# Optimization experiments

Measured on AMD Instinct MI355X. Metric: run time of the kernel, lower is better.

Reference implementation:

```python
import jax, jax.numpy as jnp
import numpy as np

BATCH, SEQ, DIM = 4, 4096, 256
DT_RANK, D_STATE, NUM_TOKENS = 16, 16, 1024


def _adapool(x, T):
    # uniform window mean == AdaptiveAvgPool1d when S % T == 0
    B, S, D = x.shape
    return x.reshape(B, T, S // T, D).mean(axis=2)


def _layernorm(x, g, b, eps=1e-5):
    mu = x.mean(-1, keepdims=True)
    var = ((x - mu) ** 2).mean(-1, keepdims=True)
    return (x - mu) * jax.lax.rsqrt(var + eps) * g + b


def _gauss_mask(T):
    c = (T + 1) // 2
    idx = jnp.arange(T, dtype=jnp.float32)
    sigma = jnp.abs(idx - c).mean()
    w = jnp.exp(-0.5 * (idx - c) ** 2 / sigma ** 2)
    return w / w.sum()


def _ssm(x, Wdbc, Wdt, bdt, Alog, D):
    A = -jnp.exp(Alog)                                     # (Dm, N)
    dbc = x @ Wdbc.T                                       # (B,L,dt+2N)
    delta = jax.nn.softplus(dbc[..., :DT_RANK] @ Wdt.T + bdt)   # (B,L,Dm)
    Bm = dbc[..., DT_RANK:DT_RANK + D_STATE]               # (B,L,N)
    Cm = dbc[..., DT_RANK + D_STATE:]                      # (B,L,N)
    deltaA = jnp.exp(delta[..., None] * A)                 # (B,L,Dm,N)
    BX = (delta[..., None] * Bm[:, :, None, :]) * x[..., None]
    def comb(c1, c2):
        a1, x1 = c1
        a2, x2 = c2
        return (a2 * a1, a2 * x1 + x2)
    _, hs = jax.lax.associative_scan(comb, (deltaA, BX), axis=1)
    y = jnp.einsum('bldn,bln->bld', hs, Cm) + D * x
    return y


def setup_inputs():
    key = jax.random.key(0)
    ks = jax.random.split(key, 16)
    s = 0.05
    Alog = jnp.tile(jnp.log(jnp.arange(1.0, D_STATE + 1.0, dtype=jnp.float32))[None, :], (DIM, 1))
    return {
        'x': jax.random.normal(ks[0], (BATCH, SEQ, DIM), jnp.float32),
        'ln_g': jnp.ones((DIM,), jnp.float32),
        'ln_b': jnp.zeros((DIM,), jnp.float32),
        'W1': jax.random.normal(ks[1], (DIM, DIM), jnp.float32) * s,
        'b1': jnp.zeros((DIM,), jnp.float32),
        'W2': jax.random.normal(ks[2], (DIM, DIM), jnp.float32) * s,
        'b2': jnp.zeros((DIM,), jnp.float32),
        'Wcf': jax.random.normal(ks[3], (DIM, DIM), jnp.float32) * s,
        'bcf': jnp.zeros((DIM,), jnp.float32),
        'Wcb': jax.random.normal(ks[4], (DIM, DIM), jnp.float32) * s,
        'bcb': jnp.zeros((DIM,), jnp.float32),
        'Wdbc_f': jax.random.normal(ks[5], (DT_RANK + 2 * D_STATE, DIM), jnp.float32) * s,
        'Wdt_f': jax.random.normal(ks[6], (DIM, DT_RANK), jnp.float32) * s,
        'bdt_f': jnp.zeros((DIM,), jnp.float32),
        'Alog_f': Alog,
        'D_f': jnp.ones((DIM,), jnp.float32),
        'Wdbc_b': jax.random.normal(ks[7], (DT_RANK + 2 * D_STATE, DIM), jnp.float32) * s,
        'Wdt_b': jax.random.normal(ks[8], (DIM, DT_RANK), jnp.float32) * s,
        'bdt_b': jnp.zeros((DIM,), jnp.float32),
        'Alog_b': Alog,
        'D_b': jnp.ones((DIM,), jnp.float32),
    }


def reference(x, ln_g, ln_b, W1, b1, W2, b2, Wcf, bcf, Wcb, bcb,
              Wdbc_f, Wdt_f, bdt_f, Alog_f, D_f,
              Wdbc_b, Wdt_b, bdt_b, Alog_b, D_b):
    skip = _adapool(x, NUM_TOKENS)
    xn = _layernorm(x, ln_g, ln_b)
    z = xn @ W1.T + b1
    xp = xn @ W2.T + b2
    mask = _gauss_mask(NUM_TOKENS)[None, :, None]

    # forward direction: 1x1 conv (= channel linear) -> softplus -> SSM
    h1 = jax.nn.softplus(jnp.einsum('bsd,ed->bse', xp, Wcf) + bcf)
    x1 = _ssm(h1, Wdbc_f, Wdt_f, bdt_f, Alog_f, D_f)
    x1 = jax.nn.silu(_adapool(x1, NUM_TOKENS) * mask)

    # backward direction on flipped sequence
    h2 = jax.nn.softplus(jnp.einsum('bsd,ed->bse', xp[:, ::-1], Wcb) + bcb)
    x2 = _ssm(h2, Wdbc_b, Wdt_b, bdt_b, Alog_b, D_b)[:, ::-1]
    x2 = jax.nn.silu(_adapool(x2, NUM_TOKENS) * mask)

    zp = jax.nn.silu(_adapool(z, NUM_TOKENS))
    return zp * x1 + zp * x2 + skip
```

## Files before the change

### kernel.cpp

```cpp
#include <hip/hip_runtime.h>
#include <math.h>


namespace {
constexpr int BB = 4;
constexpr int LL = 4096;
constexpr int DD = 256;
constexpr int NS = 16;
constexpr int NCH = 64;
constexpr int CLEN = 64;
constexpr int TOK = 1024;

constexpr size_t NROW = (size_t)BB * LL;
constexpr size_t NE   = NROW * DD;
constexpr size_t NP   = (size_t)BB * TOK * DD;
constexpr size_t NBC  = NROW * NS;
constexpr size_t NAGG = 2ull * BB * DD * NCH * NS;

constexpr size_t O_XN   = 0;
constexpr size_t O_DLF  = O_XN;
constexpr size_t O_DLB  = NE / 2;
constexpr size_t O_H1X  = NE;
constexpr size_t O_G2X  = NE + NE / 2;
constexpr size_t O_BMF  = 2 * NE;
constexpr size_t O_CMF  = O_BMF + NBC / 2;
constexpr size_t O_BMB  = O_CMF + NBC / 2;
constexpr size_t O_CMB  = O_BMB + NBC / 2;
constexpr size_t O_ZP   = O_CMB + NBC / 2;
constexpr size_t O_SKIP = O_ZP + NP;
constexpr size_t O_Y1   = O_SKIP + NP;
constexpr size_t O_Y2   = O_Y1 + NP;
constexpr size_t O_WF1  = O_Y2 + NP;
constexpr size_t O_BF1  = O_WF1 + 768 * 256 / 2;
constexpr size_t O_WF2F = O_BF1 + 768;
constexpr size_t O_B2F  = O_WF2F + 384 * 256 / 2;
constexpr size_t O_WF2B = O_B2F + 384;
constexpr size_t O_B2B  = O_WF2B + 384 * 256 / 2;
constexpr size_t O_APROD = O_B2B + 384;
constexpr size_t O_HEND = O_APROD + NAGG;
constexpr size_t O_MASK = O_HEND + NAGG;
}

typedef __bf16 bf16x8 __attribute__((ext_vector_type(8)));
typedef float f32x4 __attribute__((ext_vector_type(4)));

__device__ __forceinline__ float softplusf(float x) {
    return fmaxf(x, 0.f) + __logf(1.f + __expf(-fabsf(x)));
}
__device__ __forceinline__ float siluf(float x) {
    return x / (1.f + __expf(-x));
}
__device__ __forceinline__ void gl_lds16(const void* g, void* l) {
    __builtin_amdgcn_global_load_lds((const __attribute__((address_space(1))) unsigned int*)g,
                                     (__attribute__((address_space(3))) unsigned int*)l, 16, 0, 0);
}
__device__ __forceinline__ void pow_chain(float e1, float* p) {
    p[0] = e1;
    p[1] = e1 * e1;
    p[2] = p[1] * e1;
    p[3] = p[1] * p[1];
    p[4] = p[3] * p[0];
    p[5] = p[3] * p[1];
    p[6] = p[3] * p[2];
    p[7] = p[3] * p[3];
    p[8]  = p[7] * p[0];
    p[9]  = p[7] * p[1];
    p[10] = p[7] * p[2];
    p[11] = p[7] * p[3];
    p[12] = p[7] * p[4];
    p[13] = p[7] * p[5];
    p[14] = p[7] * p[6];
    p[15] = p[7] * p[7];
}

__global__ __launch_bounds__(256) void prep_wc_kernel(
    const float* __restrict__ W1, const float* __restrict__ b1,
    const float* __restrict__ W2, const float* __restrict__ b2,
    const float* __restrict__ Wcf, const float* __restrict__ bcf,
    const float* __restrict__ Wcb, const float* __restrict__ bcb,
    __bf16* __restrict__ Wf1, float* __restrict__ bf1)
{
    int j = blockIdx.x, mat = blockIdx.y, k = threadIdx.x;
    const float* Wc = mat ? Wcb : Wcf;
    float acc = 0.f, accb = 0.f;
    for (int m = 0; m < 256; ++m) {
        float w = Wc[j * 256 + m];
        acc  = fmaf(w, W2[m * 256 + k], acc);
        accb = fmaf(w, b2[m], accb);
    }
    Wf1[(size_t)(256 + mat * 256 + j) * 256 + k] = (__bf16)acc;
    if (k == 0) bf1[256 + mat * 256 + j] = accb + (mat ? bcb[j] : bcf[j]);
    if (mat == 0) {
        Wf1[(size_t)j * 256 + k] = (__bf16)W1[j * 256 + k];
        if (k == 0) bf1[j] = b1[j];
    }
}

__global__ __launch_bounds__(256) void prep_wdd_kernel(
    const float* __restrict__ Wdt_f, const float* __restrict__ Wdbc_f, const float* __restrict__ bdt_f,
    const float* __restrict__ Wdt_b, const float* __restrict__ Wdbc_b, const float* __restrict__ bdt_b,
    __bf16* __restrict__ Wf2f, float* __restrict__ b2f,
    __bf16* __restrict__ Wf2b, float* __restrict__ b2b)
{
    int j = blockIdx.x, mat = blockIdx.y, k = threadIdx.x;
    const float* Wdt  = mat ? Wdt_b : Wdt_f;
    const float* Wdbc = mat ? Wdbc_b : Wdbc_f;
    const float* bdt  = mat ? bdt_b : bdt_f;
    __bf16* Wf2 = mat ? Wf2b : Wf2f;
    float* b2x  = mat ? b2b : b2f;
    float val;
    if (j < 256) {
        float acc = 0.f;
#pragma unroll
        for (int m = 0; m < 16; ++m)
            acc = fmaf(Wdt[j * 16 + m], Wdbc[m * 256 + k], acc);
        val = acc;
    } else if (j < 288) {
        val = Wdbc[(16 + (j - 256)) * 256 + k];
    } else {
        val = 0.f;
    }
    Wf2[(size_t)j * 256 + k] = (__bf16)val;
    if (k == 0) b2x[j] = (j < 256) ? bdt[j] : 0.f;
}

__global__ __launch_bounds__(1024) void mask_kernel(float* __restrict__ mask)
{
    __shared__ float red[16];
    __shared__ float bc;
    int t = threadIdx.x;
    const float c = 512.f;
    float ft = (float)t;
    float v = fabsf(ft - c);
    for (int o = 32; o > 0; o >>= 1) v += __shfl_xor(v, o, 64);
    if ((t & 63) == 0) red[t >> 6] = v;
    __syncthreads();
    if (t == 0) { float s = 0; for (int i = 0; i < 16; ++i) s += red[i]; bc = s * (1.f / 1024.f); }
    __syncthreads();
    float sigma = bc;
    float w = __expf(-0.5f * (ft - c) * (ft - c) / (sigma * sigma));
    v = w;
    for (int o = 32; o > 0; o >>= 1) v += __shfl_xor(v, o, 64);
    if ((t & 63) == 0) red[t >> 6] = v;
    __syncthreads();
    if (t == 0) { float s = 0; for (int i = 0; i < 16; ++i) s += red[i]; bc = s; }
    __syncthreads();
    mask[t] = w / bc;
}

__global__ __launch_bounds__(256) void ln_kernel(
    const float* __restrict__ x, const float* __restrict__ lng, const float* __restrict__ lnb,
    __bf16* __restrict__ xn, float* __restrict__ skipo)
{
    __shared__ float red[8];
    __shared__ float mv[2];
    int t = threadIdx.x;
    int r0 = blockIdx.x * 4;
    float gg = lng[t], bbv = lnb[t];
    float acc = 0.f;
    for (int i = 0; i < 4; ++i) {
        size_t r = r0 + i;
        float v = x[r * 256 + t];
        float s = v, q = v * v;
        for (int o = 32; o > 0; o >>= 1) { s += __shfl_xor(s, o, 64); q += __shfl_xor(q, o, 64); }
        if ((t & 63) == 0) { red[t >> 6] = s; red[4 + (t >> 6)] = q; }
        __syncthreads();
        if (t == 0) {
            float S = red[0] + red[1] + red[2] + red[3];
            float Q = red[4] + red[5] + red[6] + red[7];
            float mu = S * (1.f / 256.f);
            mv[0] = mu;
            mv[1] = rsqrtf(Q * (1.f / 256.f) - mu * mu + 1e-5f);
        }
        __syncthreads();
        xn[r * 256 + t] = (__bf16)((v - mv[0]) * mv[1] * gg + bbv);
        acc += v;
        __syncthreads();
    }
    int b = r0 >> 12;
    int g = (r0 & 4095) >> 2;
    skipo[((size_t)b * TOK + g) * 256 + t] = acc * 0.25f;
}

__global__ __launch_bounds__(256) void gemm1_mfma(
    const __bf16* __restrict__ A, const __bf16* __restrict__ Bw, const float* __restrict__ bias,
    float* __restrict__ zp, __bf16* __restrict__ h1x, __bf16* __restrict__ g2x)
{
    __shared__ __align__(16) __bf16 As[4096];
    __shared__ __align__(16) __bf16 Bs[4096];
    int tid = threadIdx.x;
    int lane = tid & 63, wv = tid >> 6;
    int wr = wv >> 1, wc = wv & 1;
    int lm = lane & 15, lq = lane >> 4;
    int m0 = blockIdx.x << 7, n0 = blockIdx.y << 7;

    const __bf16* ga0 = A  + (size_t)(m0 + wv * 32 + lm) * 256 + lq * 8;
    const __bf16* ga1 = ga0 + 16 * 256;
    const __bf16* gb0 = Bw + (size_t)(n0 + wv * 32 + lm) * 256 + lq * 8;
    const __bf16* gb1 = gb0 + 16 * 256;
    __bf16* la0 = &As[(wv * 2    ) * 512];
    __bf16* la1 = &As[(wv * 2 + 1) * 512];
    __bf16* lb0 = &Bs[(wv * 2    ) * 512];
    __bf16* lb1 = &Bs[(wv * 2 + 1) * 512];

    f32x4 acc[4][4];
#pragma unroll
    for (int i = 0; i < 4; ++i)
#pragma unroll
        for (int j = 0; j < 4; ++j) acc[i][j] = 0;

    for (int k0 = 0; k0 < 256; k0 += 32) {
        __syncthreads();
        gl_lds16(ga0 + k0, la0);
        gl_lds16(ga1 + k0, la1);
        gl_lds16(gb0 + k0, lb0);
        gl_lds16(gb1 + k0, lb1);
        __syncthreads();
        bf16x8 af[4], bfr[4];
#pragma unroll
        for (int i = 0; i < 4; ++i)
            af[i] = *(const bf16x8*)&As[(wr * 4 + i) * 512 + lane * 8];
#pragma unroll
        for (int j = 0; j < 4; ++j)
            bfr[j] = *(const bf16x8*)&Bs[(wc * 4 + j) * 512 + lane * 8];
#pragma unroll
        for (int i = 0; i < 4; ++i)
#pragma unroll
            for (int j = 0; j < 4; ++j)
                acc[i][j] = __builtin_amdgcn_mfma_f32_16x16x32_bf16(af[i], bfr[j], acc[i][j], 0, 0, 0);
    }

    int target = blockIdx.y >> 1;
    if (target == 0) {
#pragma unroll
        for (int j = 0; j < 4; ++j) {
            int col = n0 + wc * 64 + j * 16 + lm;
            float bv = bias[col];
#pragma unroll
            for (int i = 0; i < 4; ++i) {
                int row0 = m0 + wr * 64 + i * 16 + lq * 4;
                float s = acc[i][j][0] + acc[i][j][1] + acc[i][j][2] + acc[i][j][3];
                float zv = siluf(0.25f * s + bv);
                int b = row0 >> 12, g = (row0 & 4095) >> 2;
                zp[((size_t)b * TOK + g) * 256 + col] = zv;
            }
        }
    } else {
        __bf16* outp = (target == 1) ? h1x : g2x;
#pragma unroll
        for (int j = 0; j < 4; ++j) {
            int col = n0 + wc * 64 + j * 16 + lm;
            float bv = bias[col];
            int cl = col & 255;
#pragma unroll
            for (int i = 0; i < 4; ++i) {
                int row = m0 + wr * 64 + i * 16 + lq * 4;
#pragma unroll
                for (int r = 0; r < 4; ++r) {
                    float v = acc[i][j][r] + bv;
                    outp[(size_t)(row + r) * 256 + cl] = (__bf16)softplusf(v);
                }
            }
        }
    }
}

__global__ __launch_bounds__(256) void gemm2_mfma(
    const __bf16* __restrict__ h1x, const __bf16* __restrict__ g2x,
    const __bf16* __restrict__ Wf, const float* __restrict__ bf2,
    const __bf16* __restrict__ Wb, const float* __restrict__ bb2,
    __bf16* __restrict__ dlf, __bf16* __restrict__ dlb,
    __bf16* __restrict__ BmF, __bf16* __restrict__ CmF,
    __bf16* __restrict__ BmB, __bf16* __restrict__ CmB)
{
    __shared__ __align__(16) __bf16 As[4096];
    __shared__ __align__(16) __bf16 Bs[4096];
    int tid = threadIdx.x;
    int lane = tid & 63, wv = tid >> 6;
    int wr = wv >> 1, wc = wv & 1;
    int lm = lane & 15, lq = lane >> 4;
    int m0 = blockIdx.x << 7, n0 = blockIdx.y << 7;
    int dir = blockIdx.z;
    const __bf16* A    = dir ? g2x : h1x;
    const __bf16* Bw   = dir ? Wb : Wf;
    const float* bias  = dir ? bb2 : bf2;
    __bf16* dl = dir ? dlb : dlf;
    __bf16* Bm = dir ? BmB : BmF;
    __bf16* Cm = dir ? CmB : CmF;

    const __bf16* ga0 = A  + (size_t)(m0 + wv * 32 + lm) * 256 + lq * 8;
    const __bf16* ga1 = ga0 + 16 * 256;
    const __bf16* gb0 = Bw + (size_t)(n0 + wv * 32 + lm) * 256 + lq * 8;
    const __bf16* gb1 = gb0 + 16 * 256;
    __bf16* la0 = &As[(wv * 2    ) * 512];
    __bf16* la1 = &As[(wv * 2 + 1) * 512];
    __bf16* lb0 = &Bs[(wv * 2    ) * 512];
    __bf16* lb1 = &Bs[(wv * 2 + 1) * 512];

    f32x4 acc[4][4];
#pragma unroll
    for (int i = 0; i < 4; ++i)
#pragma unroll
        for (int j = 0; j < 4; ++j) acc[i][j] = 0;

    for (int k0 = 0; k0 < 256; k0 += 32) {
        __syncthreads();
        gl_lds16(ga0 + k0, la0);
        gl_lds16(ga1 + k0, la1);
        gl_lds16(gb0 + k0, lb0);
        gl_lds16(gb1 + k0, lb1);
        __syncthreads();
        bf16x8 af[4], bfr[4];
#pragma unroll
        for (int i = 0; i < 4; ++i)
            af[i] = *(const bf16x8*)&As[(wr * 4 + i) * 512 + lane * 8];
#pragma unroll
        for (int j = 0; j < 4; ++j)
            bfr[j] = *(const bf16x8*)&Bs[(wc * 4 + j) * 512 + lane * 8];
#pragma unroll
        for (int i = 0; i < 4; ++i)
#pragma unroll
            for (int j = 0; j < 4; ++j)
                acc[i][j] = __builtin_amdgcn_mfma_f32_16x16x32_bf16(af[i], bfr[j], acc[i][j], 0, 0, 0);
    }

#pragma unroll
    for (int j = 0; j < 4; ++j) {
        int col = n0 + wc * 64 + j * 16 + lm;
        if (col >= 288) continue;
        float bv = bias[col];
#pragma unroll
        for (int i = 0; i < 4; ++i) {
            int row = m0 + wr * 64 + i * 16 + lq * 4;
#pragma unroll
            for (int r = 0; r < 4; ++r) {
                float v = acc[i][j][r] + bv;
                size_t rr = (size_t)(row + r);
                if (col < 256)       dl[rr * 256 + col] = (__bf16)softplusf(v);
                else if (col < 272)  Bm[rr * 16 + (col - 256)] = (__bf16)v;
                else                 Cm[rr * 16 + (col - 272)] = (__bf16)v;
            }
        }
    }
}

__global__ __launch_bounds__(256) void scan1_kernel(
    const __bf16* __restrict__ df, const __bf16* __restrict__ db,
    const __bf16* __restrict__ xf, const __bf16* __restrict__ xb,
    const __bf16* __restrict__ bmf, const __bf16* __restrict__ bmb,
    const float* __restrict__ alogf, const float* __restrict__ alogb,
    float* __restrict__ aprod, float* __restrict__ hend)
{
    int d = threadIdx.x;
    int c = blockIdx.x, b = blockIdx.y, dir = blockIdx.z;
    const __bf16* delta = dir ? db : df;
    const __bf16* xin   = dir ? xb : xf;
    const __bf16* Bm    = dir ? bmb : bmf;
    const float* Alog   = dir ? alogb : alogf;

    float A[16];
    bool intOK = true;
#pragma unroll
    for (int n = 0; n < 16; ++n) {
        A[n] = -__expf(Alog[(size_t)d * 16 + n]);
        intOK = intOK && (fabsf(A[n] + (float)(n + 1)) < 1e-3f);
    }
    float h[16];
#pragma unroll
    for (int n = 0; n < 16; ++n) h[n] = 0.f;
    float sd = 0.f;
    int base = c * CLEN;
    if (intOK) {
        for (int it = 0; it < CLEN; ++it) {
            int t = dir ? (base + CLEN - 1 - it) : (base + it);
            size_t row = (size_t)b * LL + t;
            float dlt = (float)delta[row * DD + d];
            float xv  = (float)xin[row * DD + d];
            float common = dlt * xv;
            sd += dlt;
            float p[16];
            pow_chain(__expf(-dlt), p);
            const bf16x8* Bp = (const bf16x8*)&Bm[row * NS];
            bf16x8 b0 = Bp[0], b1 = Bp[1];
#pragma unroll
            for (int n = 0; n < 8; ++n) {
                h[n]     = fmaf(p[n],     h[n],     common * (float)b0[n]);
                h[n + 8] = fmaf(p[n + 8], h[n + 8], common * (float)b1[n]);
            }
        }
        float pe[16];
        pow_chain(__expf(-sd), pe);
        size_t idx = ((((size_t)dir * BB + b) * DD + d) * NCH + c) * NS;
#pragma unroll
        for (int q = 0; q < 4; ++q) {
            float4 av, hv;
            av.x = pe[q * 4 + 0]; av.y = pe[q * 4 + 1]; av.z = pe[q * 4 + 2]; av.w = pe[q * 4 + 3];
            hv.x = h[q * 4 + 0];  hv.y = h[q * 4 + 1];  hv.z = h[q * 4 + 2];  hv.w = h[q * 4 + 3];
            *(float4*)&aprod[idx + q * 4] = av;
            *(float4*)&hend[idx + q * 4] = hv;
        }
    } else {
        for (int it = 0; it < CLEN; ++it) {
            int t = dir ? (base + CLEN - 1 - it) : (base + it);
            size_t row = (size_t)b * LL + t;
            float dlt = (float)delta[row * DD + d];
            float xv  = (float)xin[row * DD + d];
            float common = dlt * xv;
            sd += dlt;
            const bf16x8* Bp = (const bf16x8*)&Bm[row * NS];
            bf16x8 b0 = Bp[0], b1 = Bp[1];
#pragma unroll
            for (int n = 0; n < 8; ++n) {
                h[n]     = fmaf(__expf(dlt * A[n]),     h[n],     common * (float)b0[n]);
                h[n + 8] = fmaf(__expf(dlt * A[n + 8]), h[n + 8], common * (float)b1[n]);
            }
        }
        size_t idx = ((((size_t)dir * BB + b) * DD + d) * NCH + c) * NS;
#pragma unroll
        for (int n = 0; n < 16; ++n) {
            aprod[idx + n] = __expf(sd * A[n]);
            hend[idx + n] = h[n];
        }
    }
}

__global__ __launch_bounds__(256) void scan2_kernel(
    const float* __restrict__ aprod, float* __restrict__ hh)
{
    int g = blockIdx.x * 256 + threadIdx.x;
    int n = g & 15, d = (g >> 4) & 255, b = (g >> 12) & 3, dir = (g >> 14) & 1;
    size_t bidx = (((size_t)dir * BB + b) * DD + d) * NCH;
    float s = 0.f;
    if (!dir) {
        for (int c = 0; c < NCH; ++c) {
            size_t idx = (bidx + c) * NS + n;
            float a = aprod[idx], he = hh[idx];
            hh[idx] = s;
            s = fmaf(a, s, he);
        }
    } else {
        for (int c = NCH - 1; c >= 0; --c) {
            size_t idx = (bidx + c) * NS + n;
            float a = aprod[idx], he = hh[idx];
            hh[idx] = s;
            s = fmaf(a, s, he);
        }
    }
}

__global__ __launch_bounds__(256) void scan3_kernel(
    const __bf16* __restrict__ df, const __bf16* __restrict__ db,
    const __bf16* __restrict__ xf, const __bf16* __restrict__ xb,
    const __bf16* __restrict__ bmf, const __bf16* __restrict__ bmb,
    const __bf16* __restrict__ cmf, const __bf16* __restrict__ cmb,
    const float* __restrict__ alogf, const float* __restrict__ alogb,
    const float* __restrict__ Dfp, const float* __restrict__ Dbp,
    const float* __restrict__ hin,
    float* __restrict__ y1, float* __restrict__ y2)
{
    int d = threadIdx.x;
    int c = blockIdx.x, b = blockIdx.y, dir = blockIdx.z;
    const __bf16* delta = dir ? db : df;
    const __bf16* xin   = dir ? xb : xf;
    const __bf16* Bm    = dir ? bmb : bmf;
    const __bf16* Cm    = dir ? cmb : cmf;
    const float* Alog   = dir ? alogb : alogf;
    const float* Dv     = dir ? Dbp : Dfp;
    float* yout = dir ? y2 : y1;

    float A[16];
    bool intOK = true;
#pragma unroll
    for (int n = 0; n < 16; ++n) {
        A[n] = -__expf(Alog[(size_t)d * 16 + n]);
        intOK = intOK && (fabsf(A[n] + (float)(n + 1)) < 1e-3f);
    }
    float Dd = Dv[d];
    float h[16];
    size_t idx = ((((size_t)dir * BB + b) * DD + d) * NCH + c) * NS;
#pragma unroll
    for (int q = 0; q < 4; ++q) {
        float4 hv = *(const float4*)&hin[idx + q * 4];
        h[q * 4 + 0] = hv.x; h[q * 4 + 1] = hv.y; h[q * 4 + 2] = hv.z; h[q * 4 + 3] = hv.w;
    }
    int base = c * CLEN;
    float pool = 0.f;
    if (intOK) {
        for (int it = 0; it < CLEN; ++it) {
            int t = dir ? (base + CLEN - 1 - it) : (base + it);
            size_t row = (size_t)b * LL + t;
            float dlt = (float)delta[row * DD + d];
            float xv  = (float)xin[row * DD + d];
            float common = dlt * xv;
            float p[16];
            pow_chain(__expf(-dlt), p);
            const bf16x8* Bp = (const bf16x8*)&Bm[row * NS];
            const bf16x8* Cp = (const bf16x8*)&Cm[row * NS];
            bf16x8 b0 = Bp[0], b1 = Bp[1];
            bf16x8 c0 = Cp[0], c1 = Cp[1];
            float yac = 0.f;
#pragma unroll
            for (int n = 0; n < 8; ++n) {
                h[n]     = fmaf(p[n],     h[n],     common * (float)b0[n]);
                h[n + 8] = fmaf(p[n + 8], h[n + 8], common * (float)b1[n]);
                yac = fmaf(h[n], (float)c0[n], yac);
                yac = fmaf(h[n + 8], (float)c1[n], yac);
            }
            pool += yac + Dd * xv;
            bool gend = dir ? ((t & 3) == 0) : ((t & 3) == 3);
            if (gend) {
                yout[((size_t)b * TOK + (t >> 2)) * DD + d] = pool * 0.25f;
                pool = 0.f;
            }
        }
    } else {
        for (int it = 0; it < CLEN; ++it) {
            int t = dir ? (base + CLEN - 1 - it) : (base + it);
            size_t row = (size_t)b * LL + t;
            float dlt = (float)delta[row * DD + d];
            float xv  = (float)xin[row * DD + d];
            float common = dlt * xv;
            const bf16x8* Bp = (const bf16x8*)&Bm[row * NS];
            const bf16x8* Cp = (const bf16x8*)&Cm[row * NS];
            bf16x8 b0 = Bp[0], b1 = Bp[1];
            bf16x8 c0 = Cp[0], c1 = Cp[1];
            float yac = 0.f;
#pragma unroll
            for (int n = 0; n < 8; ++n) {
                h[n]     = fmaf(__expf(dlt * A[n]),     h[n],     common * (float)b0[n]);
                h[n + 8] = fmaf(__expf(dlt * A[n + 8]), h[n + 8], common * (float)b1[n]);
                yac = fmaf(h[n], (float)c0[n], yac);
                yac = fmaf(h[n + 8], (float)c1[n], yac);
            }
            pool += yac + Dd * xv;
            bool gend = dir ? ((t & 3) == 0) : ((t & 3) == 3);
            if (gend) {
                yout[((size_t)b * TOK + (t >> 2)) * DD + d] = pool * 0.25f;
                pool = 0.f;
            }
        }
    }
}

__global__ __launch_bounds__(256) void final_kernel(
    const float* __restrict__ zp, const float* __restrict__ y1, const float* __restrict__ y2,
    const float* __restrict__ mask, const float* __restrict__ skipi, float* __restrict__ out)
{
    int p = blockIdx.x;
    int g = p & 1023;
    int d = threadIdx.x;
    size_t ip = (size_t)p * 256 + d;
    float mk = mask[g];
    float a1 = y1[ip] * mk, a2 = y2[ip] * mk;
    out[ip] = zp[ip] * (siluf(a1) + siluf(a2)) + skipi[ip];
}

extern "C" void kernel_launch(void* const* d_in, const int* in_sizes, int n_in,
                              void* d_out, int out_size, void* d_ws, size_t ws_size,
                              hipStream_t stream)
{
    const float* x      = (const float*)d_in[0];
    const float* ln_g   = (const float*)d_in[1];
    const float* ln_b   = (const float*)d_in[2];
    const float* W1     = (const float*)d_in[3];
    const float* b1     = (const float*)d_in[4];
    const float* W2     = (const float*)d_in[5];
    const float* b2     = (const float*)d_in[6];
    const float* Wcf    = (const float*)d_in[7];
    const float* bcf    = (const float*)d_in[8];
    const float* Wcb    = (const float*)d_in[9];
    const float* bcb    = (const float*)d_in[10];
    const float* Wdbc_f = (const float*)d_in[11];
    const float* Wdt_f  = (const float*)d_in[12];
    const float* bdt_f  = (const float*)d_in[13];
    const float* Alog_f = (const float*)d_in[14];
    const float* D_f    = (const float*)d_in[15];
    const float* Wdbc_b = (const float*)d_in[16];
    const float* Wdt_b  = (const float*)d_in[17];
    const float* bdt_b  = (const float*)d_in[18];
    const float* Alog_b = (const float*)d_in[19];
    const float* D_b    = (const float*)d_in[20];
    float* out = (float*)d_out;
    float* ws  = (float*)d_ws;

    __bf16* xnb = (__bf16*)(ws + O_XN);
    __bf16* dlf = (__bf16*)(ws + O_DLF);
    __bf16* dlb = (__bf16*)(ws + O_DLB);
    __bf16* h1x = (__bf16*)(ws + O_H1X);
    __bf16* g2x = (__bf16*)(ws + O_G2X);
    __bf16* bmf = (__bf16*)(ws + O_BMF);
    __bf16* cmf = (__bf16*)(ws + O_CMF);
    __bf16* bmb = (__bf16*)(ws + O_BMB);
    __bf16* cmb = (__bf16*)(ws + O_CMB);
    float* zpb  = ws + O_ZP;
    float* skb  = ws + O_SKIP;
    float* y1b  = ws + O_Y1;
    float* y2b  = ws + O_Y2;
    __bf16* wf1 = (__bf16*)(ws + O_WF1);
    float* bf1  = ws + O_BF1;
    __bf16* wf2f = (__bf16*)(ws + O_WF2F);
    float* b2f  = ws + O_B2F;
    __bf16* wf2b = (__bf16*)(ws + O_WF2B);
    float* b2b  = ws + O_B2B;
    float* apr  = ws + O_APROD;
    float* hnd  = ws + O_HEND;
    float* mkb  = ws + O_MASK;

    prep_wc_kernel<<<dim3(256, 2), 256, 0, stream>>>(W1, b1, W2, b2, Wcf, bcf, Wcb, bcb, wf1, bf1);
    prep_wdd_kernel<<<dim3(384, 2), 256, 0, stream>>>(Wdt_f, Wdbc_f, bdt_f, Wdt_b, Wdbc_b, bdt_b,
                                                      wf2f, b2f, wf2b, b2b);
    mask_kernel<<<1, 1024, 0, stream>>>(mkb);
    ln_kernel<<<4096, 256, 0, stream>>>(x, ln_g, ln_b, xnb, skb);
    gemm1_mfma<<<dim3(128, 6), 256, 0, stream>>>(xnb, wf1, bf1, zpb, h1x, g2x);
    gemm2_mfma<<<dim3(128, 3, 2), 256, 0, stream>>>(h1x, g2x, wf2f, b2f, wf2b, b2b,
                                                    dlf, dlb, bmf, cmf, bmb, cmb);
    scan1_kernel<<<dim3(NCH, BB, 2), 256, 0, stream>>>(dlf, dlb, h1x, g2x, bmf, bmb,
                                                       Alog_f, Alog_b, apr, hnd);
    scan2_kernel<<<128, 256, 0, stream>>>(apr, hnd);
    scan3_kernel<<<dim3(NCH, BB, 2), 256, 0, stream>>>(dlf, dlb, h1x, g2x, bmf, bmb, cmf, cmb,
                                                       Alog_f, Alog_b, D_f, D_b, hnd, y1b, y2b);
    final_kernel<<<4096, 256, 0, stream>>>(zpb, y1b, y2b, mkb, skb, out);
}
```

Measured before the change: 252.2 us.

## Stage GEMM epilogues through LDS for vectorized stores and merge prep kernels

The GEMM1 and GEMM2 epilogues now write their activated results into a padded shared-memory staging tile and then store them to global memory as 16-byte vectors. This replaces the scattered per-element 2-byte and 4-byte stores that came straight out of the MFMA register layout. The three weight-prep and mask kernels are merged into one launch, with the Gaussian mask sigma folded into a constant. The scan2 loops are also unrolled. The extra shared memory per block can lower occupancy, and the staging adds extra barriers.

```diff
diff --git a/kernel.cpp b/kernel.cpp
--- a/kernel.cpp
+++ b/kernel.cpp
@@ -39,6 +39,8 @@
 constexpr size_t O_APROD = O_B2B + 384;
 constexpr size_t O_HEND = O_APROD + NAGG;
 constexpr size_t O_MASK = O_HEND + NAGG;
+
+constexpr int SSTRIDE = 136;
 }
 
 typedef __bf16 bf16x8 __attribute__((ext_vector_type(8)));
@@ -73,79 +75,75 @@
     p[15] = p[7] * p[7];
 }
 
-__global__ __launch_bounds__(256) void prep_wc_kernel(
+__global__ __launch_bounds__(256) void prep_all_kernel(
     const float* __restrict__ W1, const float* __restrict__ b1,
     const float* __restrict__ W2, const float* __restrict__ b2,
     const float* __restrict__ Wcf, const float* __restrict__ bcf,
     const float* __restrict__ Wcb, const float* __restrict__ bcb,
-    __bf16* __restrict__ Wf1, float* __restrict__ bf1)
-{
-    int j = blockIdx.x, mat = blockIdx.y, k = threadIdx.x;
-    const float* Wc = mat ? Wcb : Wcf;
-    float acc = 0.f, accb = 0.f;
-    for (int m = 0; m < 256; ++m) {
-        float w = Wc[j * 256 + m];
-        acc  = fmaf(w, W2[m * 256 + k], acc);
-        accb = fmaf(w, b2[m], accb);
-    }
-    Wf1[(size_t)(256 + mat * 256 + j) * 256 + k] = (__bf16)acc;
-    if (k == 0) bf1[256 + mat * 256 + j] = accb + (mat ? bcb[j] : bcf[j]);
-    if (mat == 0) {
-        Wf1[(size_t)j * 256 + k] = (__bf16)W1[j * 256 + k];
-        if (k == 0) bf1[j] = b1[j];
-    }
-}
-
-__global__ __launch_bounds__(256) void prep_wdd_kernel(
     const float* __restrict__ Wdt_f, const float* __restrict__ Wdbc_f, const float* __restrict__ bdt_f,
     const float* __restrict__ Wdt_b, const float* __restrict__ Wdbc_b, const float* __restrict__ bdt_b,
+    __bf16* __restrict__ Wf1, float* __restrict__ bf1,
     __bf16* __restrict__ Wf2f, float* __restrict__ b2f,
-    __bf16* __restrict__ Wf2b, float* __restrict__ b2b)
-{
-    int j = blockIdx.x, mat = blockIdx.y, k = threadIdx.x;
-    const float* Wdt  = mat ? Wdt_b : Wdt_f;
-    const float* Wdbc = mat ? Wdbc_b : Wdbc_f;
-    const float* bdt  = mat ? bdt_b : bdt_f;
-    __bf16* Wf2 = mat ? Wf2b : Wf2f;
-    float* b2x  = mat ? b2b : b2f;
-    float val;
-    if (j < 256) {
-        float acc = 0.f;
-#pragma unroll
-        for (int m = 0; m < 16; ++m)
-            acc = fmaf(Wdt[j * 16 + m], Wdbc[m * 256 + k], acc);
-        val = acc;
-    } else if (j < 288) {
-        val = Wdbc[(16 + (j - 256)) * 256 + k];
-    } else {
-        val = 0.f;
-    }
-    Wf2[(size_t)j * 256 + k] = (__bf16)val;
-    if (k == 0) b2x[j] = (j < 256) ? bdt[j] : 0.f;
-}
-
-__global__ __launch_bounds__(1024) void mask_kernel(float* __restrict__ mask)
-{
-    __shared__ float red[16];
-    __shared__ float bc;
-    int t = threadIdx.x;
-    const float c = 512.f;
-    float ft = (float)t;
-    float v = fabsf(ft - c);
-    for (int o = 32; o > 0; o >>= 1) v += __shfl_xor(v, o, 64);
-    if ((t & 63) == 0) red[t >> 6] = v;
-    __syncthreads();
-    if (t == 0) { float s = 0; for (int i = 0; i < 16; ++i) s += red[i]; bc = s * (1.f / 1024.f); }
-    __syncthreads();
-    float sigma = bc;
-    float w = __expf(-0.5f * (ft - c) * (ft - c) / (sigma * sigma));
-    v = w;
-    for (int o = 32; o > 0; o >>= 1) v += __shfl_xor(v, o, 64);
-    if ((t & 63) == 0) red[t >> 6] = v;
-    __syncthreads();
-    if (t == 0) { float s = 0; for (int i = 0; i < 16; ++i) s += red[i]; bc = s; }
-    __syncthreads();
-    mask[t] = w / bc;
+    __bf16* __restrict__ Wf2b, float* __restrict__ b2b,
+    float* __restrict__ mask)
+{
+    int bx = blockIdx.x, mat = blockIdx.y, k = threadIdx.x;
+    if (bx < 256) {
+        int j = bx;
+        const float* Wc = mat ? Wcb : Wcf;
+        float acc = 0.f, accb = 0.f;
+        for (int m = 0; m < 256; ++m) {
+            float w = Wc[j * 256 + m];
+            acc  = fmaf(w, W2[m * 256 + k], acc);
+            accb = fmaf(w, b2[m], accb);
+        }
+        Wf1[(size_t)(256 + mat * 256 + j) * 256 + k] = (__bf16)acc;
+        if (k == 0) bf1[256 + mat * 256 + j] = accb + (mat ? bcb[j] : bcf[j]);
+        if (mat == 0) {
+            Wf1[(size_t)j * 256 + k] = (__bf16)W1[j * 256 + k];
+            if (k == 0) bf1[j] = b1[j];
+        }
+    } else if (bx < 640) {
+        int j = bx - 256;
+        const float* Wdt  = mat ? Wdt_b : Wdt_f;
+        const float* Wdbc = mat ? Wdbc_b : Wdbc_f;
+        const float* bdt  = mat ? bdt_b : bdt_f;
+        __bf16* Wf2 = mat ? Wf2b : Wf2f;
+        float* b2x  = mat ? b2b : b2f;
+        float val;
+        if (j < 256) {
+            float acc = 0.f;
+#pragma unroll
+            for (int m = 0; m < 16; ++m)
+                acc = fmaf(Wdt[j * 16 + m], Wdbc[m * 256 + k], acc);
+            val = acc;
+        } else if (j < 288) {
+            val = Wdbc[(16 + (j - 256)) * 256 + k];
+        } else {
+            val = 0.f;
+        }
+        Wf2[(size_t)j * 256 + k] = (__bf16)val;
+        if (k == 0) b2x[j] = (j < 256) ? bdt[j] : 0.f;
+    } else if (mat == 0) {
+        __shared__ float red[4];
+        __shared__ float sb;
+        float w[4];
+        float loc = 0.f;
+#pragma unroll
+        for (int q = 0; q < 4; ++q) {
+            float dd = (float)(k + 256 * q) - 512.f;
+            w[q] = __expf(-0.5f * dd * dd * (1.f / 65536.f));
+            loc += w[q];
+        }
+        for (int o = 32; o > 0; o >>= 1) loc += __shfl_xor(loc, o, 64);
+        if ((k & 63) == 0) red[k >> 6] = loc;
+        __syncthreads();
+        if (k == 0) sb = red[0] + red[1] + red[2] + red[3];
+        __syncthreads();
+        float inv = 1.f / sb;
+#pragma unroll
+        for (int q = 0; q < 4; ++q) mask[k + 256 * q] = w[q] * inv;
+    }
 }
 
 __global__ __launch_bounds__(256) void ln_kernel(
@@ -188,6 +186,7 @@
 {
     __shared__ __align__(16) __bf16 As[4096];
     __shared__ __align__(16) __bf16 Bs[4096];
+    __shared__ __align__(16) unsigned char Stage[128 * SSTRIDE * 2];
     int tid = threadIdx.x;
     int lane = tid & 63, wv = tid >> 6;
     int wr = wv >> 1, wc = wv & 1;
@@ -231,36 +230,54 @@
     }
 
     int target = blockIdx.y >> 1;
+    int colbase = (blockIdx.y & 1) * 128;
+    __syncthreads();
     if (target == 0) {
+        float* zs = (float*)Stage;
 #pragma unroll
         for (int j = 0; j < 4; ++j) {
-            int col = n0 + wc * 64 + j * 16 + lm;
-            float bv = bias[col];
+            int coll = wc * 64 + j * 16 + lm;
+            float bv = bias[n0 + coll];
 #pragma unroll
             for (int i = 0; i < 4; ++i) {
-                int row0 = m0 + wr * 64 + i * 16 + lq * 4;
+                int gl = wr * 16 + i * 4 + lq;
                 float s = acc[i][j][0] + acc[i][j][1] + acc[i][j][2] + acc[i][j][3];
-                float zv = siluf(0.25f * s + bv);
-                int b = row0 >> 12, g = (row0 & 4095) >> 2;
-                zp[((size_t)b * TOK + g) * 256 + col] = zv;
-            }
+                zs[gl * 132 + coll] = siluf(0.25f * s + bv);
+            }
+        }
+        __syncthreads();
+        int b = m0 >> 12, g0 = (m0 & 4095) >> 2;
+        int rl = tid >> 5;
+        int c4 = (tid & 31) * 4;
+#pragma unroll
+        for (int p = 0; p < 4; ++p) {
+            int g = p * 8 + rl;
+            float4 v = *(float4*)&zs[g * 132 + c4];
+            *(float4*)&zp[((size_t)b * TOK + g0 + g) * 256 + colbase + c4] = v;
         }
     } else {
+        __bf16* hs = (__bf16*)Stage;
+#pragma unroll
+        for (int j = 0; j < 4; ++j) {
+            int coll = wc * 64 + j * 16 + lm;
+            float bv = bias[n0 + coll];
+#pragma unroll
+            for (int i = 0; i < 4; ++i) {
+                int rl = wr * 64 + i * 16 + lq * 4;
+#pragma unroll
+                for (int r = 0; r < 4; ++r)
+                    hs[(rl + r) * SSTRIDE + coll] = (__bf16)softplusf(acc[i][j][r] + bv);
+            }
+        }
+        __syncthreads();
         __bf16* outp = (target == 1) ? h1x : g2x;
-#pragma unroll
-        for (int j = 0; j < 4; ++j) {
-            int col = n0 + wc * 64 + j * 16 + lm;
-            float bv = bias[col];
-            int cl = col & 255;
-#pragma unroll
-            for (int i = 0; i < 4; ++i) {
-                int row = m0 + wr * 64 + i * 16 + lq * 4;
-#pragma unroll
-                for (int r = 0; r < 4; ++r) {
-                    float v = acc[i][j][r] + bv;
-                    outp[(size_t)(row + r) * 256 + cl] = (__bf16)softplusf(v);
-                }
-            }
+        int rl = tid >> 4;
+        int c8 = (tid & 15) * 8;
+#pragma unroll
+        for (int p = 0; p < 8; ++p) {
+            int row = p * 16 + rl;
+            bf16x8 v = *(bf16x8*)&hs[row * SSTRIDE + c8];
+            *(bf16x8*)&outp[(size_t)(m0 + row) * 256 + colbase + c8] = v;
         }
     }
 }
@@ -275,6 +292,7 @@
 {
     __shared__ __align__(16) __bf16 As[4096];
     __shared__ __align__(16) __bf16 Bs[4096];
+    __shared__ __align__(16) unsigned char Stage[128 * SSTRIDE * 2];
     int tid = threadIdx.x;
     int lane = tid & 63, wv = tid >> 6;
     int wr = wv >> 1, wc = wv & 1;
@@ -324,23 +342,56 @@
                 acc[i][j] = __builtin_amdgcn_mfma_f32_16x16x32_bf16(af[i], bfr[j], acc[i][j], 0, 0, 0);
     }
 
-#pragma unroll
-    for (int j = 0; j < 4; ++j) {
-        int col = n0 + wc * 64 + j * 16 + lm;
-        if (col >= 288) continue;
-        float bv = bias[col];
-#pragma unroll
-        for (int i = 0; i < 4; ++i) {
-            int row = m0 + wr * 64 + i * 16 + lq * 4;
-#pragma unroll
-            for (int r = 0; r < 4; ++r) {
-                float v = acc[i][j][r] + bv;
-                size_t rr = (size_t)(row + r);
-                if (col < 256)       dl[rr * 256 + col] = (__bf16)softplusf(v);
-                else if (col < 272)  Bm[rr * 16 + (col - 256)] = (__bf16)v;
-                else                 Cm[rr * 16 + (col - 272)] = (__bf16)v;
-            }
-        }
+    __syncthreads();
+    if (blockIdx.y < 2) {
+        __bf16* hs = (__bf16*)Stage;
+        int colbase = (blockIdx.y & 1) * 128;
+#pragma unroll
+        for (int j = 0; j < 4; ++j) {
+            int coll = wc * 64 + j * 16 + lm;
+            float bv = bias[n0 + coll];
+#pragma unroll
+            for (int i = 0; i < 4; ++i) {
+                int rl = wr * 64 + i * 16 + lq * 4;
+#pragma unroll
+                for (int r = 0; r < 4; ++r)
+                    hs[(rl + r) * SSTRIDE + coll] = (__bf16)softplusf(acc[i][j][r] + bv);
+            }
+        }
+        __syncthreads();
+        int rl = tid >> 4;
+        int c8 = (tid & 15) * 8;
+#pragma unroll
+        for (int p = 0; p < 8; ++p) {
+            int row = p * 16 + rl;
+            bf16x8 v = *(bf16x8*)&hs[row * SSTRIDE + c8];
+            *(bf16x8*)&dl[(size_t)(m0 + row) * 256 + colbase + c8] = v;
+        }
+    } else {
+        __bf16* bs_ = (__bf16*)Stage;
+        __bf16* cs_ = (__bf16*)Stage + 128 * 24;
+        if (wc == 0) {
+#pragma unroll
+            for (int j = 0; j < 2; ++j) {
+                int coll = j * 16 + lm;
+                float bv = bias[n0 + coll];
+                __bf16* dst = j ? cs_ : bs_;
+#pragma unroll
+                for (int i = 0; i < 4; ++i) {
+                    int rl = wr * 64 + i * 16 + lq * 4;
+#pragma unroll
+                    for (int r = 0; r < 4; ++r)
+                        dst[(rl + r) * 24 + lm] = (__bf16)(acc[i][j][r] + bv);
+                }
+            }
+        }
+        __syncthreads();
+        int row = tid >> 1;
+        int c8 = (tid & 1) * 8;
+        bf16x8 vb = *(bf16x8*)&bs_[row * 24 + c8];
+        bf16x8 vc = *(bf16x8*)&cs_[row * 24 + c8];
+        *(bf16x8*)&Bm[(size_t)(m0 + row) * 16 + c8] = vb;
+        *(bf16x8*)&Cm[(size_t)(m0 + row) * 16 + c8] = vc;
     }
 }
 
@@ -432,6 +483,7 @@
     size_t bidx = (((size_t)dir * BB + b) * DD + d) * NCH;
     float s = 0.f;
     if (!dir) {
+#pragma unroll 8
         for (int c = 0; c < NCH; ++c) {
             size_t idx = (bidx + c) * NS + n;
             float a = aprod[idx], he = hh[idx];
@@ -439,6 +491,7 @@
             s = fmaf(a, s, he);
         }
     } else {
+#pragma unroll 8
         for (int c = NCH - 1; c >= 0; --c) {
             size_t idx = (bidx + c) * NS + n;
             float a = aprod[idx], he = hh[idx];
@@ -606,10 +659,10 @@
     float* hnd  = ws + O_HEND;
     float* mkb  = ws + O_MASK;
 
-    prep_wc_kernel<<<dim3(256, 2), 256, 0, stream>>>(W1, b1, W2, b2, Wcf, bcf, Wcb, bcb, wf1, bf1);
-    prep_wdd_kernel<<<dim3(384, 2), 256, 0, stream>>>(Wdt_f, Wdbc_f, bdt_f, Wdt_b, Wdbc_b, bdt_b,
-                                                      wf2f, b2f, wf2b, b2b);
-    mask_kernel<<<1, 1024, 0, stream>>>(mkb);
+    prep_all_kernel<<<dim3(641, 2), 256, 0, stream>>>(
+        W1, b1, W2, b2, Wcf, bcf, Wcb, bcb,
+        Wdt_f, Wdbc_f, bdt_f, Wdt_b, Wdbc_b, bdt_b,
+        wf1, bf1, wf2f, b2f, wf2b, b2b, mkb);
     ln_kernel<<<4096, 256, 0, stream>>>(x, ln_g, ln_b, xnb, skb);
     gemm1_mfma<<<dim3(128, 6), 256, 0, stream>>>(xnb, wf1, bf1, zpb, h1x, g2x);
     gemm2_mfma<<<dim3(128, 3, 2), 256, 0, stream>>>(h1x, g2x, wf2f, b2f, wf2b, b2b,
```

New measurement: 243.0 us. -3.6%, faster.
